# Optimization experiments

Measured on AMD Instinct MI355X. Metric: run time of the kernel, lower is better.

## Reference

```python
import jax, jax.numpy as jnp
import numpy as np
jax.config.update("jax_enable_x64", True)  # hashing uses int64 primes as in torch

N_PTS = 1048576
L, T, F = 16, 2 ** 18, 2
N_MIN, N_MAX = 16, 1024
HID, OUT = 64, 3


def setup_inputs() -> dict:
    key = jax.random.key(0)
    ks = jax.random.split(key, 6)
    X = jax.random.uniform(ks[0], (N_PTS, 2), dtype=jnp.float32)
    hash_table = jax.random.uniform(ks[1], (L, T, F), dtype=jnp.float32,
                                    minval=-1e-4, maxval=1e-4)
    def lin(k, fan_in, fan_out):
        bound = 1.0 / np.sqrt(fan_in)
        kw, kb = jax.random.split(k)
        W = jax.random.uniform(kw, (fan_in, fan_out), dtype=jnp.float32,
                               minval=-bound, maxval=bound)
        b = jax.random.uniform(kb, (fan_out,), dtype=jnp.float32,
                               minval=-bound, maxval=bound)
        return W, b
    W1, b1 = lin(ks[2], L * F, HID)
    W2, b2 = lin(ks[3], HID, HID)
    W3, b3 = lin(ks[4], HID, HID)
    W4, b4 = lin(ks[5], HID, OUT)
    return {"X": X, "hash_table": hash_table,
            "W1": W1, "b1": b1, "W2": W2, "b2": b2,
            "W3": W3, "b3": b3, "W4": W4, "b4": b4}


def reference(X, hash_table, W1, b1, W2, b2, W3, b3, W4, b4):
    Lh, Th, Fh = hash_table.shape
    # per-level resolutions: floor(N_min * b**l), b geometric between N_min and N_max
    b_geo = np.exp((np.log(N_MAX) - np.log(N_MIN)) / (Lh - 1))
    N_values = jnp.floor(jnp.asarray(N_MIN * b_geo ** np.arange(Lh),
                                     dtype=jnp.float32))  # (L,)

    x_scaled = X[:, :, None] * N_values[None, None, :]        # (N, 2, L)
    x_floor = jnp.floor(x_scaled)

    # NOTE: original code MULTIPLIES floor coords by the 0/1 vertex pattern
    # (not add) -- we replicate that math faithfully.
    vertices = jnp.array([[0., 0., 1., 1.], [0., 1., 0., 1.]],
                         dtype=jnp.float32)                   # (2, 4)
    x_vert = (x_floor[:, :, :, None] * vertices[None, :, None, :]
              ).astype(jnp.int64)                             # (N, 2, L, 4)

    primes = jnp.array([1, 2654435761], dtype=jnp.int64)
    hv = x_vert * primes[None, :, None, None]
    x_hash = jnp.remainder(jnp.bitwise_xor(hv[:, 0], hv[:, 1]), Th)  # (N, L, 4)

    # irregular gather: per-level hash table lookup -> (N, L, 4, F)
    lookup = hash_table[jnp.arange(Lh)[None, :, None], x_hash]

    w = x_scaled - x_floor                                    # (N, 2, L)
    fx, fy = w[:, 0, :], w[:, 1, :]
    cx, cy = 1.0 - fx, 1.0 - fy
    f_stack = jnp.stack([cx * cy, cx * fy, fx * cy, fx * fy], axis=2)  # (N, L, 4)

    x_interp = jnp.sum(f_stack[:, :, :, None] * lookup, axis=2)  # (N, L, F)
    feat = x_interp.reshape(-1, Lh * Fh).astype(jnp.float32)     # (N, 32)

    h = jax.nn.leaky_relu(feat @ W1 + b1)
    h = jax.nn.leaky_relu(h @ W2 + b2)
    h = jax.nn.leaky_relu(h @ W3 + b3)
    return jax.nn.relu(h @ W4 + b4)
```

## Files before the change

kernel.cpp:

```cpp
#include <hip/hip_runtime.h>
#include <math.h>

typedef _Float16 half8  __attribute__((ext_vector_type(8)));
typedef _Float16 half2v __attribute__((ext_vector_type(2)));
typedef float    float4v __attribute__((ext_vector_type(4)));

constexpr int T_ = 1 << 18;
constexpr unsigned TMASK = T_ - 1;
constexpr unsigned PRIME = 2654435761u;
constexpr int HP = 72;

constexpr int WFRAG_HALFS = 22 * 64 * 8;
constexpr int BIAS_FLOATS = 208;
constexpr int WS_BYTES    = 22528 + 240 * 4;
constexpr int WS_UINT4    = WS_BYTES / 16;
constexpr int MAX_STAGE   = 4224;

constexpr int BLK   = 512;
constexpr int WAVES = 8;
constexpr int PTS_PER_BLOCK = 1024;

struct Meta { float n[16]; float off[16]; };

__global__ void prep_weights(const float* __restrict__ W1, const float* __restrict__ b1,
                             const float* __restrict__ W2, const float* __restrict__ b2,
                             const float* __restrict__ W3, const float* __restrict__ b3,
                             const float* __restrict__ W4, const float* __restrict__ b4,
                             _Float16* __restrict__ wsW, float* __restrict__ wsB, Meta mv)
{
    const int tid = threadIdx.x;
    if (blockIdx.x < 44) {
        const int e = blockIdx.x * 256 + tid;
        const int frag = e >> 9;
        const int l    = (e >> 3) & 63;
        const int j    = e & 7;
        const int g = l >> 4, m = l & 15;
        float v;
        if (frag < 4) {
            v = W1[(8*g + j) * 64 + 16*frag + m];
        } else if (frag < 12) {
            const int s = (frag - 4) >> 2, t = (frag - 4) & 3;
            v = W2[(32*s + 8*g + j) * 64 + 16*t + m];
        } else if (frag < 20) {
            const int s = (frag - 12) >> 2, t = (frag - 12) & 3;
            v = W3[(32*s + 8*g + j) * 64 + 16*t + m];
        } else {
            const int s = frag - 20;
            v = (m < 3) ? W4[(32*s + 8*g + j) * 3 + m] : 0.f;
        }
        wsW[e] = (_Float16)v;
    } else {
        if (tid < 64) { wsB[tid] = b1[tid]; wsB[64 + tid] = b2[tid]; wsB[128 + tid] = b3[tid]; }
        else if (tid < 80)  { const int r = tid - 64; wsB[192 + r] = (r < 3) ? b4[r] : 0.f; }
        else if (tid < 96)  wsB[BIAS_FLOATS + (tid - 80)] = mv.n[tid - 80];
        else if (tid < 112) wsB[BIAS_FLOATS + 16 + (tid - 96)] = mv.off[tid - 96];
    }
}

#define DS_FENCE() __asm__ volatile("s_waitcnt lgkmcnt(0)" ::: "memory")

__device__ __forceinline__ void issue_v3(float2 (&v3)[4], const float2 xy,
                                         const float2* __restrict__ table,
                                         const float (&nvq)[4], const int g)
{
    #pragma unroll
    for (int q = 0; q < 4; ++q) {
        const float n = nvq[q];
        const float xs = xy.x * n, ys = xy.y * n;
        const unsigned xi = (unsigned)(int)floorf(xs);
        const unsigned yi = (unsigned)(int)floorf(ys);
        v3[q] = table[(size_t)(4*g + q) * T_ + ((xi ^ (yi * PRIME)) & TMASK)];
    }
}

__device__ __forceinline__ half8 make_feat(const float2 xy, const float2 (&v3)[4],
                                           const float (&nvq)[4], const int (&offq)[4],
                                           const half2v* __restrict__ sV1,
                                           const half2v* __restrict__ sV2,
                                           const float2 (&v0c)[4])
{
    half8 feat;
    #pragma unroll
    for (int q = 0; q < 4; ++q) {
        const float n = nvq[q];
        const float xs = xy.x * n, ys = xy.y * n;
        const float xf = floorf(xs), yf = floorf(ys);
        const float fx = xs - xf, fy = ys - yf;
        const int xi = (int)xf, yi = (int)yf;
        const half2v v1h = sV1[offq[q] + yi];
        const half2v v2h = sV2[offq[q] + xi];
        const float cx = 1.f - fx, cy = 1.f - fy;
        const float w0 = cx*cy, w1 = cx*fy, w2 = fx*cy, w3 = fx*fy;
        feat[2*q+0] = (_Float16)(w0*v0c[q].x + w1*(float)v1h[0] + w2*(float)v2h[0] + w3*v3[q].x);
        feat[2*q+1] = (_Float16)(w0*v0c[q].y + w1*(float)v1h[1] + w2*(float)v2h[1] + w3*v3[q].y);
    }
    return feat;
}

__device__ __forceinline__ void act_store(_Float16* __restrict__ H, const int c,
                                          const int g, const int t, const float4v acc)
{
    union { _Float16 h[4]; float2 f2; } u;
    #pragma unroll
    for (int r = 0; r < 4; ++r) {
        const float v = acc[r];
        u.h[r] = (_Float16)(v > 0.f ? v : 0.01f * v);
    }
    *(float2*)(H + c*HP + 16*t + 4*g) = u.f2;
}

__global__ __launch_bounds__(BLK)
void fused_hashnerf_mfma(const float2* __restrict__ X,
                         const float2* __restrict__ table,
                         const uint4* __restrict__ ws,
                         float* __restrict__ out)
{
    __shared__ uint4    sRaw[WS_UINT4];
    __shared__ _Float16 sH[WAVES][16 * HP];
    __shared__ half2v   sV1[MAX_STAGE];
    __shared__ half2v   sV2[MAX_STAGE];

    const int tid = threadIdx.x;
    for (int i = tid; i < WS_UINT4; i += BLK) sRaw[i] = ws[i];
    __syncthreads();

    const _Float16* Wl = (const _Float16*)sRaw;
    const float*    Bl = (const float*)(sRaw + (22528 / 16));

    {
        const float* NVp = Bl + BIAS_FLOATS;
        const float* OFp = Bl + BIAS_FLOATS + 16;
        for (int l = 0; l < 16; ++l) {
            const int nl  = (int)NVp[l];
            const int off = (int)OFp[l];
            const float2* tl = table + (size_t)l * T_;
            for (int i = tid; i <= nl; i += BLK) {
                const float2 a = tl[i];
                const float2 b = tl[((unsigned)i * PRIME) & TMASK];
                sV2[off + i] = half2v{(_Float16)a.x, (_Float16)a.y};
                sV1[off + i] = half2v{(_Float16)b.x, (_Float16)b.y};
            }
        }
    }
    __syncthreads();

    const int wave = tid >> 6, lane = tid & 63;
    const int g = lane >> 4, c = lane & 15;
    _Float16* H = &sH[wave][0];

    float4v b1f[4], b2f[4], b3f[4], b4f;
    #pragma unroll
    for (int t = 0; t < 4; ++t) {
        b1f[t] = *(const float4v*)(Bl +       16*t + 4*g);
        b2f[t] = *(const float4v*)(Bl +  64 + 16*t + 4*g);
        b3f[t] = *(const float4v*)(Bl + 128 + 16*t + 4*g);
    }
    b4f = *(const float4v*)(Bl + 192 + 4*g);
    float nvq[4];
    int   offq[4];
    #pragma unroll
    for (int q = 0; q < 4; ++q) {
        nvq[q]  = Bl[BIAS_FLOATS + 4*g + q];
        offq[q] = (int)Bl[BIAS_FLOATS + 16 + 4*g + q];
    }

    const int base_pt = blockIdx.x * PTS_PER_BLOCK + wave * 128;

    float2 xy[8];
    #pragma unroll
    for (int it = 0; it < 8; ++it) xy[it] = X[base_pt + it*16 + c];

    float2 v0c[4];
    #pragma unroll
    for (int q = 0; q < 4; ++q) v0c[q] = table[(size_t)(4*g + q) * T_];

    float2 GA[4], GB[4];
    issue_v3(GA, xy[0], table, nvq, g);

    #pragma unroll
    for (int it = 0; it < 8; ++it) {
        float2 (&Gc)[4] = (it & 1) ? GB : GA;
        float2 (&Gn)[4] = (it & 1) ? GA : GB;

        const half8 feat = make_feat(xy[it], Gc, nvq, offq, sV1, sV2, v0c);

        if (it < 7) issue_v3(Gn, xy[it+1], table, nvq, g);
        __builtin_amdgcn_sched_barrier(0);

        float4v acc[4];
        #pragma unroll
        for (int t = 0; t < 4; ++t) {
            const half8 wf = *(const half8*)(Wl + (t*64 + lane)*8);
            acc[t] = __builtin_amdgcn_mfma_f32_16x16x32_f16(wf, feat, b1f[t], 0, 0, 0);
        }
        #pragma unroll
        for (int t = 0; t < 4; ++t) act_store(H, c, g, t, acc[t]);
        DS_FENCE();

        half8 a0 = *(const half8*)(H + c*HP +      8*g);
        half8 a1 = *(const half8*)(H + c*HP + 32 + 8*g);
        #pragma unroll
        for (int t = 0; t < 4; ++t) {
            const half8 w0f = *(const half8*)(Wl + ((4 + t)*64 + lane)*8);
            const half8 w1f = *(const half8*)(Wl + ((8 + t)*64 + lane)*8);
            float4v a = __builtin_amdgcn_mfma_f32_16x16x32_f16(w0f, a0, b2f[t], 0, 0, 0);
            acc[t]    = __builtin_amdgcn_mfma_f32_16x16x32_f16(w1f, a1, a,      0, 0, 0);
        }
        #pragma unroll
        for (int t = 0; t < 4; ++t) act_store(H, c, g, t, acc[t]);
        DS_FENCE();

        a0 = *(const half8*)(H + c*HP +      8*g);
        a1 = *(const half8*)(H + c*HP + 32 + 8*g);
        #pragma unroll
        for (int t = 0; t < 4; ++t) {
            const half8 w0f = *(const half8*)(Wl + ((12 + t)*64 + lane)*8);
            const half8 w1f = *(const half8*)(Wl + ((16 + t)*64 + lane)*8);
            float4v a = __builtin_amdgcn_mfma_f32_16x16x32_f16(w0f, a0, b3f[t], 0, 0, 0);
            acc[t]    = __builtin_amdgcn_mfma_f32_16x16x32_f16(w1f, a1, a,      0, 0, 0);
        }
        #pragma unroll
        for (int t = 0; t < 4; ++t) act_store(H, c, g, t, acc[t]);
        DS_FENCE();

        a0 = *(const half8*)(H + c*HP +      8*g);
        a1 = *(const half8*)(H + c*HP + 32 + 8*g);
        const half8 w40 = *(const half8*)(Wl + (20*64 + lane)*8);
        const half8 w41 = *(const half8*)(Wl + (21*64 + lane)*8);
        float4v o = __builtin_amdgcn_mfma_f32_16x16x32_f16(w40, a0, b4f, 0, 0, 0);
        o         = __builtin_amdgcn_mfma_f32_16x16x32_f16(w41, a1, o,   0, 0, 0);
        if (g == 0) {
            float* op = out + (size_t)3 * (base_pt + it * 16 + c);
            op[0] = fmaxf(o[0], 0.f);
            op[1] = fmaxf(o[1], 0.f);
            op[2] = fmaxf(o[2], 0.f);
        }
    }
}

extern "C" void kernel_launch(void* const* d_in, const int* in_sizes, int n_in,
                              void* d_out, int out_size, void* d_ws, size_t ws_size,
                              hipStream_t stream) {
    const float2* X     = (const float2*)d_in[0];
    const float2* table = (const float2*)d_in[1];
    const float*  W1    = (const float*)d_in[2];
    const float*  b1    = (const float*)d_in[3];
    const float*  W2    = (const float*)d_in[4];
    const float*  b2    = (const float*)d_in[5];
    const float*  W3    = (const float*)d_in[6];
    const float*  b3    = (const float*)d_in[7];
    const float*  W4    = (const float*)d_in[8];
    const float*  b4    = (const float*)d_in[9];
    float* out          = (float*)d_out;

    const int npts = in_sizes[0] / 2;

    Meta mv;
    const double bg = exp((log(1024.0) - log(16.0)) / 15.0);
    int acc = 0;
    for (int l = 0; l < 16; ++l) {
        const float nl = floorf((float)(16.0 * pow(bg, (double)l)));
        mv.n[l]   = nl;
        mv.off[l] = (float)acc;
        acc += (int)nl + 1;
    }

    _Float16* wsW = (_Float16*)d_ws;
    float*    wsB = (float*)((char*)d_ws + 22528);

    prep_weights<<<45, 256, 0, stream>>>(W1, b1, W2, b2, W3, b3, W4, b4, wsW, wsB, mv);
    fused_hashnerf_mfma<<<npts / PTS_PER_BLOCK, BLK, 0, stream>>>(X, table, (const uint4*)d_ws, out);
}
```

Baseline: 215.5 us.

## Precompute axis-vertex table slices once in workspace, gather from global instead of LDS

The per-block staging of the v1/v2 vertex values (the hashed entries where one coordinate is zero) into shared memory is removed. The prep kernel now builds one packed fp16 array of those values in the workspace, and the main kernel gathers them from global memory alongside the v3 gather, prefetched one iteration ahead. This removes the redundant per-block table loads and the extra barrier, and frees about 34KB of LDS so launch_bounds can ask for 2 blocks per CU. In exchange each point issues extra global loads, which should mostly hit in cache.

```diff
diff --git a/kernel.cpp b/kernel.cpp
--- a/kernel.cpp
+++ b/kernel.cpp
@@ -14,6 +14,7 @@
 constexpr int BIAS_FLOATS = 208;
 constexpr int WS_BYTES    = 22528 + 240 * 4;
 constexpr int WS_UINT4    = WS_BYTES / 16;
+constexpr int V12_OFF     = 23488;
 constexpr int MAX_STAGE   = 4224;
 
 constexpr int BLK   = 512;
@@ -26,11 +27,14 @@
                              const float* __restrict__ W2, const float* __restrict__ b2,
                              const float* __restrict__ W3, const float* __restrict__ b3,
                              const float* __restrict__ W4, const float* __restrict__ b4,
-                             _Float16* __restrict__ wsW, float* __restrict__ wsB, Meta mv)
+                             const float2* __restrict__ table,
+                             _Float16* __restrict__ wsW, float* __restrict__ wsB,
+                             uint2* __restrict__ wsV, Meta mv)
 {
     const int tid = threadIdx.x;
-    if (blockIdx.x < 44) {
-        const int e = blockIdx.x * 256 + tid;
+    const int bid = blockIdx.x;
+    if (bid < 44) {
+        const int e = bid * 256 + tid;
         const int frag = e >> 9;
         const int l    = (e >> 3) & 63;
         const int j    = e & 7;
@@ -49,34 +53,59 @@
             v = (m < 3) ? W4[(32*s + 8*g + j) * 3 + m] : 0.f;
         }
         wsW[e] = (_Float16)v;
-    } else {
+    } else if (bid == 44) {
         if (tid < 64) { wsB[tid] = b1[tid]; wsB[64 + tid] = b2[tid]; wsB[128 + tid] = b3[tid]; }
         else if (tid < 80)  { const int r = tid - 64; wsB[192 + r] = (r < 3) ? b4[r] : 0.f; }
         else if (tid < 96)  wsB[BIAS_FLOATS + (tid - 80)] = mv.n[tid - 80];
         else if (tid < 112) wsB[BIAS_FLOATS + 16 + (tid - 96)] = mv.off[tid - 96];
+    } else {
+        const int e = (bid - 45) * 256 + tid;
+        const int total = (int)mv.off[15] + (int)mv.n[15] + 1;
+        if (e < total) {
+            int l = 0;
+            #pragma unroll
+            for (int k = 1; k < 16; ++k) if (e >= (int)mv.off[k]) l = k;
+            const int i = e - (int)mv.off[l];
+            const float2* tl = table + (size_t)l * T_;
+            const float2 b = tl[((unsigned)i * PRIME) & TMASK];
+            const float2 a = tl[i];
+            union { _Float16 h[2]; unsigned u; } p0, p1;
+            p0.h[0] = (_Float16)b.x; p0.h[1] = (_Float16)b.y;
+            p1.h[0] = (_Float16)a.x; p1.h[1] = (_Float16)a.y;
+            wsV[e] = uint2{p0.u, p1.u};
+        }
     }
 }
 
 #define DS_FENCE() __asm__ volatile("s_waitcnt lgkmcnt(0)" ::: "memory")
 
-__device__ __forceinline__ void issue_v3(float2 (&v3)[4], const float2 xy,
-                                         const float2* __restrict__ table,
-                                         const float (&nvq)[4], const int g)
+struct Gather {
+    float2   v3[4];
+    unsigned v1[4];
+    unsigned v2[4];
+};
+
+__device__ __forceinline__ void issue_gather(Gather& G, const float2 xy,
+                                             const float2* __restrict__ table,
+                                             const unsigned* __restrict__ gV12,
+                                             const float (&nvq)[4], const int (&offq)[4],
+                                             const int g)
 {
     #pragma unroll
     for (int q = 0; q < 4; ++q) {
         const float n = nvq[q];
         const float xs = xy.x * n, ys = xy.y * n;
-        const unsigned xi = (unsigned)(int)floorf(xs);
-        const unsigned yi = (unsigned)(int)floorf(ys);
-        v3[q] = table[(size_t)(4*g + q) * T_ + ((xi ^ (yi * PRIME)) & TMASK)];
-    }
-}
-
-__device__ __forceinline__ half8 make_feat(const float2 xy, const float2 (&v3)[4],
-                                           const float (&nvq)[4], const int (&offq)[4],
-                                           const half2v* __restrict__ sV1,
-                                           const half2v* __restrict__ sV2,
+        const int xi = (int)floorf(xs);
+        const int yi = (int)floorf(ys);
+        const unsigned yp = (unsigned)yi * PRIME;
+        G.v3[q] = table[(size_t)(4*g + q) * T_ + (((unsigned)xi ^ yp) & TMASK)];
+        G.v1[q] = gV12[2*(offq[q] + yi) + 0];
+        G.v2[q] = gV12[2*(offq[q] + xi) + 1];
+    }
+}
+
+__device__ __forceinline__ half8 make_feat(const float2 xy, const Gather& G,
+                                           const float (&nvq)[4],
                                            const float2 (&v0c)[4])
 {
     half8 feat;
@@ -86,13 +115,12 @@
         const float xs = xy.x * n, ys = xy.y * n;
         const float xf = floorf(xs), yf = floorf(ys);
         const float fx = xs - xf, fy = ys - yf;
-        const int xi = (int)xf, yi = (int)yf;
-        const half2v v1h = sV1[offq[q] + yi];
-        const half2v v2h = sV2[offq[q] + xi];
+        union { unsigned u; _Float16 h[2]; } u1, u2;
+        u1.u = G.v1[q]; u2.u = G.v2[q];
         const float cx = 1.f - fx, cy = 1.f - fy;
         const float w0 = cx*cy, w1 = cx*fy, w2 = fx*cy, w3 = fx*fy;
-        feat[2*q+0] = (_Float16)(w0*v0c[q].x + w1*(float)v1h[0] + w2*(float)v2h[0] + w3*v3[q].x);
-        feat[2*q+1] = (_Float16)(w0*v0c[q].y + w1*(float)v1h[1] + w2*(float)v2h[1] + w3*v3[q].y);
+        feat[2*q+0] = (_Float16)(w0*v0c[q].x + w1*(float)u1.h[0] + w2*(float)u2.h[0] + w3*G.v3[q].x);
+        feat[2*q+1] = (_Float16)(w0*v0c[q].y + w1*(float)u1.h[1] + w2*(float)u2.h[1] + w3*G.v3[q].y);
     }
     return feat;
 }
@@ -109,7 +137,7 @@
     *(float2*)(H + c*HP + 16*t + 4*g) = u.f2;
 }
 
-__global__ __launch_bounds__(BLK)
+__global__ __launch_bounds__(BLK, 2)
 void fused_hashnerf_mfma(const float2* __restrict__ X,
                          const float2* __restrict__ table,
                          const uint4* __restrict__ ws,
@@ -117,8 +145,6 @@
 {
     __shared__ uint4    sRaw[WS_UINT4];
     __shared__ _Float16 sH[WAVES][16 * HP];
-    __shared__ half2v   sV1[MAX_STAGE];
-    __shared__ half2v   sV2[MAX_STAGE];
 
     const int tid = threadIdx.x;
     for (int i = tid; i < WS_UINT4; i += BLK) sRaw[i] = ws[i];
@@ -126,23 +152,7 @@
 
     const _Float16* Wl = (const _Float16*)sRaw;
     const float*    Bl = (const float*)(sRaw + (22528 / 16));
-
-    {
-        const float* NVp = Bl + BIAS_FLOATS;
-        const float* OFp = Bl + BIAS_FLOATS + 16;
-        for (int l = 0; l < 16; ++l) {
-            const int nl  = (int)NVp[l];
-            const int off = (int)OFp[l];
-            const float2* tl = table + (size_t)l * T_;
-            for (int i = tid; i <= nl; i += BLK) {
-                const float2 a = tl[i];
-                const float2 b = tl[((unsigned)i * PRIME) & TMASK];
-                sV2[off + i] = half2v{(_Float16)a.x, (_Float16)a.y};
-                sV1[off + i] = half2v{(_Float16)b.x, (_Float16)b.y};
-            }
-        }
-    }
-    __syncthreads();
+    const unsigned* gV12 = (const unsigned*)((const char*)ws + V12_OFF);
 
     const int wave = tid >> 6, lane = tid & 63;
     const int g = lane >> 4, c = lane & 15;
@@ -174,17 +184,17 @@
     #pragma unroll
     for (int q = 0; q < 4; ++q) v0c[q] = table[(size_t)(4*g + q) * T_];
 
-    float2 GA[4], GB[4];
-    issue_v3(GA, xy[0], table, nvq, g);
+    Gather GA, GB;
+    issue_gather(GA, xy[0], table, gV12, nvq, offq, g);
 
     #pragma unroll
     for (int it = 0; it < 8; ++it) {
-        float2 (&Gc)[4] = (it & 1) ? GB : GA;
-        float2 (&Gn)[4] = (it & 1) ? GA : GB;
-
-        const half8 feat = make_feat(xy[it], Gc, nvq, offq, sV1, sV2, v0c);
-
-        if (it < 7) issue_v3(Gn, xy[it+1], table, nvq, g);
+        Gather& Gc = (it & 1) ? GB : GA;
+        Gather& Gn = (it & 1) ? GA : GB;
+
+        const half8 feat = make_feat(xy[it], Gc, nvq, v0c);
+
+        if (it < 7) issue_gather(Gn, xy[it+1], table, gV12, nvq, offq, g);
         __builtin_amdgcn_sched_barrier(0);
 
         float4v acc[4];
@@ -267,7 +277,9 @@
 
     _Float16* wsW = (_Float16*)d_ws;
     float*    wsB = (float*)((char*)d_ws + 22528);
-
-    prep_weights<<<45, 256, 0, stream>>>(W1, b1, W2, b2, W3, b3, W4, b4, wsW, wsB, mv);
+    uint2*    wsV = (uint2*)((char*)d_ws + V12_OFF);
+
+    prep_weights<<<62, 256, 0, stream>>>(W1, b1, W2, b2, W3, b3, W4, b4, table,
+                                         wsW, wsB, wsV, mv);
     fused_hashnerf_mfma<<<npts / PTS_PER_BLOCK, BLK, 0, stream>>>(X, table, (const uint4*)d_ws, out);
 }
```

Measured after the change: 219.1 us. About the same (+1.6%).
